# Optimization experiments

Hardware: AMD Instinct MI355X
Metric: run time of the kernel (lower is better)

## Reference

```python
import jax, jax.numpy as jnp
import numpy as np

N = 100_000   # nodes
E = 600_000   # edges
D = 128       # embed_dim
G = 1000      # graphs (batch ids)
L = 3         # num_layers


def setup_inputs() -> dict:
    key = jax.random.key(0)
    ks = jax.random.split(key, 12)
    s = 1.0 / np.sqrt(D)
    return {
        "x": jax.random.normal(ks[0], (N, D), jnp.float32),
        "edge_index": jax.random.randint(ks[1], (2, E), 0, N),
        "batch": jnp.sort(jax.random.randint(ks[2], (N,), 0, G)),
        "mask": jax.random.randint(ks[3], (N,), 0, 2),
        # stacked GCNConv weights/biases (in=hidden=out=D)
        "gcn_w": jax.random.normal(ks[4], (L, D, D), jnp.float32) * s,
        "gcn_b": jnp.zeros((L, D), jnp.float32),
        # MLP head: Linear(D,D) -> ReLU -> Linear(D,1)
        "lin1_w": jax.random.normal(ks[5], (D, D), jnp.float32) * s,
        "lin1_b": jnp.zeros((D,), jnp.float32),
        "lin2_w": jax.random.normal(ks[6], (D,), jnp.float32) * s,
        "lin2_b": jnp.zeros((), jnp.float32),
    }


def gcn_forward(x, src, dst, gcn_w, gcn_b):
    # symmetric gcn_norm with self-loops: deg[i] = 1 + in-degree(i)
    deg = jax.ops.segment_sum(jnp.ones((E,), x.dtype), dst, num_segments=N) + 1.0
    dinv = jax.lax.rsqrt(deg)
    enorm = dinv[src] * dinv[dst]          # [E] edge normalization
    self_norm = (dinv * dinv)[:, None]     # [N,1] self-loop normalization
    h = x
    for l in range(L):
        h = h @ gcn_w[l]                   # [N,D]
        h = (jax.ops.segment_sum(h[src] * enorm[:, None], dst, num_segments=N)
             + h * self_norm)
        h = h + gcn_b[l]
        if l < L - 1:
            h = jax.nn.relu(h)  # (dropout inactive at inference)
    return h


def reference(x, edge_index, batch, mask, gcn_w, gcn_b, lin1_w, lin1_b, lin2_w, lin2_b):
    src, dst = edge_index[0], edge_index[1]
    h = gcn_forward(x, src, dst, gcn_w, gcn_b)
    # MLP head -> per-node score [N]
    s = jax.nn.relu(h @ lin1_w + lin1_b) @ lin2_w + lin2_b
    s = jnp.where(mask == 0, jnp.float32(-1e9), s)
    # per-graph (segment) softmax — fused replacement for the unique/batch loop
    m = jax.ops.segment_max(s, batch, num_segments=G)
    e = jnp.exp(s - m[batch])
    z = jax.ops.segment_sum(e, batch, num_segments=G)
    return e / z[batch]
```

## Files before the change

kernel.cpp:

```cpp
#include <hip/hip_runtime.h>
#include <hip/hip_bf16.h>
#include <stdint.h>

typedef unsigned int u32;
typedef unsigned short u16;
typedef __attribute__((ext_vector_type(8))) short bf16x8;
typedef __attribute__((ext_vector_type(4))) float f32x4;

__device__ __forceinline__ float u16tof(u16 u){ return __uint_as_float(((u32)u) << 16); }
__device__ __forceinline__ float lo16(u32 v){ return __uint_as_float(v << 16); }
__device__ __forceinline__ float hi16(u32 v){ return __uint_as_float(v & 0xffff0000u); }
__device__ __forceinline__ u16 ftobf(float f){
  u32 b = __float_as_uint(f);
  return (u16)((b + 0x7FFFu + ((b >> 16) & 1u)) >> 16);
}
__device__ __forceinline__ u32 pack2(float a, float b){
  return (u32)ftobf(a) | ((u32)ftobf(b) << 16);
}
__device__ __forceinline__ float ldf(const void* p, int i, int isbf){
  return isbf ? u16tof(((const u16*)p)[i]) : ((const float*)p)[i];
}

__device__ __forceinline__ void acc8(float* a, uint4 v, float mk){
  a[0] = fmaf(lo16(v.x), mk, a[0]);
  a[1] = fmaf(hi16(v.x), mk, a[1]);
  a[2] = fmaf(lo16(v.y), mk, a[2]);
  a[3] = fmaf(hi16(v.y), mk, a[3]);
  a[4] = fmaf(lo16(v.z), mk, a[4]);
  a[5] = fmaf(hi16(v.z), mk, a[5]);
  a[6] = fmaf(lo16(v.w), mk, a[6]);
  a[7] = fmaf(hi16(v.w), mk, a[7]);
}

__device__ __forceinline__ void async16(const u16* g, const u16* l){
  __builtin_amdgcn_global_load_lds(
      (const __attribute__((address_space(1))) u32*)(uintptr_t)g,
      (__attribute__((address_space(3))) u32*)(uintptr_t)l,
      16, 0, 0);
}

__global__ __launch_bounds__(256) void k_prep(const void* __restrict__ gw, const void* __restrict__ l1w,
                                              const void* __restrict__ x, u16* __restrict__ Wf,
                                              u16* __restrict__ Hb, int L, int n8, int cvtB, int goffB,
                                              const int* __restrict__ batch, int* __restrict__ goff,
                                              int N, int G,
                                              const int* __restrict__ dst, int* __restrict__ hist,
                                              int nE, int chunk, int* __restrict__ flag){
  __shared__ int sh[256];
  const int b = blockIdx.x;
  const int t = threadIdx.x;
  const int histStart = L + 1 + cvtB + goffB;

  if (b >= histStart){
    sh[t] = 0; __syncthreads();
    const int blk = b - histStart;
    const int e0 = blk * chunk, e1 = min(e0 + chunk, nE);
    for (int e = e0 + t; e < e1; e += 256) atomicAdd(&sh[dst[e] >> 9], 1);
    __syncthreads();
    hist[blk * 256 + t] = sh[t];
    return;
  }
  if (b >= L + 1 + cvtB){
    const int i = (b - (L + 1 + cvtB)) * 256 + t;
    if (i >= N) return;
    const int bt = batch[i];
    const int prev = (i == 0) ? -1 : batch[i - 1];
    for (int g = prev + 1; g <= bt; ++g) goff[g] = i;
    if (i == N - 1){ for (int g = bt + 1; g <= G; ++g) goff[g] = N; }
    return;
  }
  if (t == 0) sh[0] = 0;
  __syncthreads();
  if (b <= L){
    int local = 0;
    for (int i = t; i < 4096; i += 256){
      u32 e = (((const u32*)gw)[i] >> 7) & 0xFFu;
      if (e >= 100u && e < 127u) local++;
    }
    atomicAdd(&sh[0], local);
    __syncthreads();
    const int isbf = (sh[0] > 2048) ? 1 : 0;
    if (b == 0 && t == 0) *flag = isbf;

    const void* src = (b < L) ? gw : l1w;
    const int sbase = (b < L) ? b * 16384 : 0;
    u16* dstp = Wf + (size_t)b * 16384;
    for (int g = t; g < 2048; g += 256){
      const int tt = g >> 8, ks = (g >> 6) & 3, lane = g & 63;
      const int n = tt * 16 + (lane & 15);
      const int k0 = ks * 32 + ((lane >> 4) << 3);
      u16* d = dstp + (size_t)g * 8;
      #pragma unroll
      for (int j = 0; j < 8; ++j){
        d[j] = ftobf(ldf(src, sbase + (k0 + j) * 128 + n, isbf));
      }
    }
  } else {
    u32 e = (((const u32*)gw)[t] >> 7) & 0xFFu;
    atomicAdd(&sh[0], (e >= 100u && e < 127u) ? 1 : 0);
    __syncthreads();
    if (sh[0] > 128) return;
    const int i = (b - (L + 1)) * 256 + t;
    if (i >= n8) return;
    const float4 a = ((const float4*)x)[i * 2];
    const float4 c = ((const float4*)x)[i * 2 + 1];
    u16* o = Hb + (size_t)i * 8;
    o[0] = ftobf(a.x); o[1] = ftobf(a.y); o[2] = ftobf(a.z); o[3] = ftobf(a.w);
    o[4] = ftobf(c.x); o[5] = ftobf(c.y); o[6] = ftobf(c.z); o[7] = ftobf(c.w);
  }
}

__global__ __launch_bounds__(256) void k_hscan(int* __restrict__ hist, int* __restrict__ bb, int nE){
  const int t = threadIdx.x;
  int run = 0;
  for (int j = 0; j < 256; j += 8){
    int v[8];
    #pragma unroll
    for (int k = 0; k < 8; ++k) v[k] = hist[(j + k) * 256 + t];
    #pragma unroll
    for (int k = 0; k < 8; ++k){
      hist[(j + k) * 256 + t] = run;
      run += v[k];
    }
  }
  __shared__ int sm[256];
  sm[t] = run; __syncthreads();
  for (int off = 1; off < 256; off <<= 1){
    int a = (t >= off) ? sm[t - off] : 0;
    __syncthreads();
    sm[t] += a;
    __syncthreads();
  }
  bb[t] = sm[t] - run;
  if (t == 255) bb[256] = nE;
}

__global__ __launch_bounds__(256) void k_scatter(const int* __restrict__ src, const int* __restrict__ dst,
                                                 const int* __restrict__ hist, const int* __restrict__ bb,
                                                 int2* __restrict__ tmpe, int nE, int chunk){
  __shared__ int base[256];
  const int blk = blockIdx.x, t = threadIdx.x;
  base[t] = bb[t] + hist[blk * 256 + t];
  __syncthreads();
  const int e0 = blk * chunk, e1 = min(e0 + chunk, nE);
  for (int e = e0 + t; e < e1; e += 256){
    const int d = dst[e];
    const int pos = atomicAdd(&base[d >> 9], 1);
    tmpe[pos] = make_int2(src[e], d);
  }
}

__global__ __launch_bounds__(256) void k_local(const int2* __restrict__ tmpe, const int* __restrict__ bb,
                                               int* __restrict__ boff, int* __restrict__ eid,
                                               float* __restrict__ dinv, int N, int nE, int nbkt){
  __shared__ int hcnt[512];
  __shared__ int hoff[512];
  const int b = blockIdx.x, t = threadIdx.x;
  const int n0 = b << 9;
  const int n1 = min(n0 + 512, N);
  const int nn = n1 - n0;
  const int e0 = bb[b], e1 = bb[b + 1];
  hcnt[t] = 0; hcnt[t + 256] = 0;
  __syncthreads();
  for (int e = e0 + t; e < e1; e += 256) atomicAdd(&hcnt[tmpe[e].y - n0], 1);
  __syncthreads();
  const int v0 = hcnt[t], v1 = hcnt[t + 256];
  hoff[t] = v0; hoff[t + 256] = v1;
  __syncthreads();
  for (int off = 1; off < 512; off <<= 1){
    int a0 = (t >= off) ? hoff[t - off] : 0;
    int a1 = (t + 256 >= off) ? hoff[t + 256 - off] : 0;
    __syncthreads();
    hoff[t] += a0; hoff[t + 256] += a1;
    __syncthreads();
  }
  const int ex0 = hoff[t] - v0 + e0;
  const int ex1 = hoff[t + 256] - v1 + e0;
  if (t < nn){       boff[n0 + t] = ex0;        dinv[n0 + t] = rsqrtf((float)v0 + 1.0f); }
  if (t + 256 < nn){ boff[n0 + t + 256] = ex1;  dinv[n0 + t + 256] = rsqrtf((float)v1 + 1.0f); }
  if (b == nbkt - 1 && t == 0) boff[N] = nE;
  __syncthreads();
  hoff[t] = ex0; hoff[t + 256] = ex1;
  __syncthreads();
  for (int e = e0 + t; e < e1; e += 256){
    const int2 pr = tmpe[e];
    const int pos = atomicAdd(&hoff[pr.y - n0], 1);
    eid[pos] = pr.x;
  }
}

__global__ __launch_bounds__(256) void k_mm(const void* __restrict__ X, const u16* __restrict__ Hb,
                                            const u16* __restrict__ Wf, const float* __restrict__ dinv,
                                            u16* __restrict__ T, int n, const int* __restrict__ fl){
  __shared__ u16 smw[16384];
  const int isbf = *fl;
  const u16* A = isbf ? (const u16*)X : Hb;
  {
    const uint4* s = (const uint4*)Wf;
    uint4* d = (uint4*)smw;
    for (int i = threadIdx.x; i < 2048; i += 256) d[i] = s[i];
  }
  __syncthreads();

  const int wave = threadIdx.x >> 6, lane = threadIdx.x & 63;
  const int m0 = blockIdx.x * 64 + wave * 16;
  int arow = m0 + (lane & 15); if (arow > n - 1) arow = n - 1;
  const u16* aptr = A + (size_t)arow * 128 + ((lane >> 4) << 3);

  f32x4 acc[8];
  #pragma unroll
  for (int t = 0; t < 8; ++t) acc[t] = (f32x4){0.f, 0.f, 0.f, 0.f};

  #pragma unroll
  for (int ks = 0; ks < 4; ++ks){
    const bf16x8 a = *(const bf16x8*)(aptr + ks * 32);
    #pragma unroll
    for (int t = 0; t < 8; ++t){
      const bf16x8 b = *(const bf16x8*)(smw + (size_t)(((t * 4 + ks) * 64 + lane) * 8));
      acc[t] = __builtin_amdgcn_mfma_f32_16x16x32_bf16(a, b, acc[t], 0, 0, 0);
    }
  }
  __syncthreads();

  const int quad = lane >> 4, col0 = lane & 15;
  float dv[4];
  #pragma unroll
  for (int r = 0; r < 4; ++r){
    const int row = m0 + quad * 4 + r;
    dv[r] = (row < n) ? dinv[row] : 0.f;
  }
  u16* my = smw + wave * 2112;
  #pragma unroll
  for (int t = 0; t < 8; ++t){
    #pragma unroll
    for (int r = 0; r < 4; ++r){
      my[(quad * 4 + r) * 132 + t * 16 + col0] = ftobf(acc[t][r] * dv[r]);
    }
  }
  #pragma unroll
  for (int i = 0; i < 4; ++i){
    const int row = i * 4 + (lane >> 4);
    const int grow = m0 + row;
    const int c8 = (lane & 15) * 8;
    if (grow < n){
      const u16* s = &my[row * 132 + c8];
      uint2 lo = *(const uint2*)(s);
      uint2 hi = *(const uint2*)(s + 4);
      *(uint4*)&T[(size_t)grow * 128 + c8] = make_uint4(lo.x, lo.y, hi.x, hi.y);
    }
  }
}

__device__ __forceinline__ void gather_ring(const u16* __restrict__ Tin, const int* __restrict__ eid,
                                            const int* __restrict__ seid, const int* __restrict__ sboff,
                                            int inlds, int e0, int wave, int lane, int sub, int l16,
                                            int js, int d, float* a){
  int T = 0;
  #pragma unroll
  for (int s = 0; s < 4; ++s){
    const int dd = sboff[wave * 4 + s + 1] - sboff[wave * 4 + s];
    T = (dd > T) ? dd : T;
  }
  if (T <= 0) return;

  if (inlds){
    extern __shared__ u16 dummy[];
    return;
  }
}

__global__ __launch_bounds__(256) void k_gmm(const u16* __restrict__ Tin, const int* __restrict__ boff,
                                             const int* __restrict__ eid, const float* __restrict__ dinv,
                                             const void* __restrict__ bias, int layer,
                                             const u16* __restrict__ Wf, u16* __restrict__ Tout,
                                             int n, const int* __restrict__ fl){
  __shared__ u16 sma[16 * 132];
  __shared__ u16 ring[4][4][512];
  __shared__ int seid[1024];
  __shared__ int sboff[17];
  const int isbf = *fl;
  const int tid = threadIdx.x;
  const int wave = tid >> 6, lane = tid & 63;
  const int sub = lane >> 4, l16 = lane & 15;
  const int m0 = blockIdx.x * 16;

  const int e0 = boff[m0];
  const int e1 = boff[min(m0 + 16, n)];
  const int len = e1 - e0;
  const int inlds = (len <= 1024);
  if (tid < 17) sboff[tid] = boff[min(m0 + tid, n)];
  if (inlds){ for (int i = tid; i < len; i += 256) seid[i] = eid[e0 + i]; }
  __syncthreads();

  const int wsub = wave * 4 + sub;
  const int node = m0 + wsub;
  const int js = sboff[wsub];
  const int d  = sboff[wsub + 1] - js;

  float a[8];
  #pragma unroll
  for (int k = 0; k < 8; ++k) a[k] = 0.f;
  if (node < n){
    const uint4 sv = ((const uint4*)(Tin + (size_t)node * 128))[l16];
    acc8(a, sv, 1.f);
  }

  int T = 0;
  #pragma unroll
  for (int s = 0; s < 4; ++s){
    const int dd = sboff[wave * 4 + s + 1] - sboff[wave * 4 + s];
    T = (dd > T) ? dd : T;
  }

  if (inlds){
    const int jloc = js - e0;
    const int jlast = jloc + ((d > 0) ? (d - 1) : 0);
    const u16* base = Tin + (size_t)l16 * 8;
    u16* slot = &ring[wave][0][0];
    #pragma unroll
    for (int t = 0; t < 4; ++t){
      if (t < T){
        const int idx = (d > 0) ? seid[(t < d) ? (jloc + t) : jlast] : 0;
        async16(base + (size_t)idx * 128, slot + (t & 3) * 512);
      }
    }
    int t = 0;
    for (; t + 4 <= T; ++t){
      asm volatile("s_waitcnt vmcnt(3)" ::: "memory");
      const uint4 v = *(const uint4*)(slot + (t & 3) * 512 + lane * 8);
      acc8(a, v, (t < d) ? 1.f : 0.f);
      const int tn = t + 4;
      if (tn < T){
        const int idx = (d > 0) ? seid[(tn < d) ? (jloc + tn) : jlast] : 0;
        async16(base + (size_t)idx * 128, slot + (tn & 3) * 512);
      }
    }
    for (; t < T; ++t){
      const int rem = T - t - 1;
      if (rem >= 2)      asm volatile("s_waitcnt vmcnt(2)" ::: "memory");
      else if (rem == 1) asm volatile("s_waitcnt vmcnt(1)" ::: "memory");
      else               asm volatile("s_waitcnt vmcnt(0)" ::: "memory");
      const uint4 v = *(const uint4*)(slot + (t & 3) * 512 + lane * 8);
      acc8(a, v, (t < d) ? 1.f : 0.f);
    }
  } else {
    for (int j = js; j < js + d; ++j){
      const uint4 v = ((const uint4*)(Tin + (size_t)eid[j] * 128))[l16];
      acc8(a, v, 1.f);
    }
  }

  float h[8];
  #pragma unroll
  for (int k = 0; k < 8; ++k) h[k] = 0.f;
  if (node < n){
    const float di = dinv[node];
    const int bb = layer * 128 + l16 * 8;
    #pragma unroll
    for (int k = 0; k < 8; ++k){
      h[k] = fmaxf(fmaf(a[k], di, ldf(bias, bb + k, isbf)), 0.f);
    }
  }
  {
    uint4 o;
    o.x = pack2(h[0], h[1]); o.y = pack2(h[2], h[3]); o.z = pack2(h[4], h[5]); o.w = pack2(h[6], h[7]);
    *(uint4*)&sma[(wave * 4 + sub) * 132 + l16 * 8] = o;
  }
  __syncthreads();

  f32x4 acc[2];
  acc[0] = (f32x4){0.f,0.f,0.f,0.f}; acc[1] = (f32x4){0.f,0.f,0.f,0.f};
  #pragma unroll
  for (int ks = 0; ks < 4; ++ks){
    const bf16x8 av = *(const bf16x8*)(sma + l16 * 132 + sub * 8 + ks * 32);
    #pragma unroll
    for (int tt = 0; tt < 2; ++tt){
      const int t = wave * 2 + tt;
      const bf16x8 bv = *(const bf16x8*)(Wf + (size_t)(((t * 4 + ks) * 64 + lane) * 8));
      acc[tt] = __builtin_amdgcn_mfma_f32_16x16x32_bf16(av, bv, acc[tt], 0, 0, 0);
    }
  }
  __syncthreads();

  float dv[4];
  #pragma unroll
  for (int r = 0; r < 4; ++r){
    const int row = m0 + sub * 4 + r;
    dv[r] = (row < n) ? dinv[row] : 0.f;
  }
  #pragma unroll
  for (int tt = 0; tt < 2; ++tt){
    const int t = wave * 2 + tt;
    #pragma unroll
    for (int r = 0; r < 4; ++r){
      sma[(sub * 4 + r) * 132 + t * 16 + l16] = ftobf(acc[tt][r] * dv[r]);
    }
  }
  __syncthreads();

  {
    const int row = tid >> 4;
    const int c8 = (tid & 15) * 8;
    if (m0 + row < n){
      const u16* s = &sma[row * 132 + c8];
      uint2 lo = *(const uint2*)(s);
      uint2 hi = *(const uint2*)(s + 4);
      *(uint4*)&Tout[(size_t)(m0 + row) * 128 + c8] = make_uint4(lo.x, lo.y, hi.x, hi.y);
    }
  }
}

__global__ __launch_bounds__(256) void k_ghead(const u16* __restrict__ Tin, const int* __restrict__ boff,
                                               const int* __restrict__ eid, const float* __restrict__ dinv,
                                               const void* __restrict__ bias, int layer,
                                               const u16* __restrict__ Wf, const void* __restrict__ b1,
                                               const void* __restrict__ w2, const void* __restrict__ b2,
                                               const int* __restrict__ mask, float* __restrict__ s,
                                               int n, const int* __restrict__ fl){
  __shared__ u16 sma[16 * 132];
  __shared__ u16 ring[4][4][512];
  __shared__ int seid[1024];
  __shared__ int sboff[17];
  __shared__ float sred[4][16];
  const int isbf = *fl;
  const int tid = threadIdx.x;
  const int wave = tid >> 6, lane = tid & 63;
  const int sub = lane >> 4, l16 = lane & 15;
  const int m0 = blockIdx.x * 16;

  const int e0 = boff[m0];
  const int e1 = boff[min(m0 + 16, n)];
  const int len = e1 - e0;
  const int inlds = (len <= 1024);
  if (tid < 17) sboff[tid] = boff[min(m0 + tid, n)];
  if (inlds){ for (int i = tid; i < len; i += 256) seid[i] = eid[e0 + i]; }
  __syncthreads();

  const int wsub = wave * 4 + sub;
  const int node = m0 + wsub;
  const int js = sboff[wsub];
  const int d  = sboff[wsub + 1] - js;

  float a[8];
  #pragma unroll
  for (int k = 0; k < 8; ++k) a[k] = 0.f;
  if (node < n){
    const uint4 sv = ((const uint4*)(Tin + (size_t)node * 128))[l16];
    acc8(a, sv, 1.f);
  }

  int T = 0;
  #pragma unroll
  for (int s2 = 0; s2 < 4; ++s2){
    const int dd = sboff[wave * 4 + s2 + 1] - sboff[wave * 4 + s2];
    T = (dd > T) ? dd : T;
  }

  if (inlds){
    const int jloc = js - e0;
    const int jlast = jloc + ((d > 0) ? (d - 1) : 0);
    const u16* base = Tin + (size_t)l16 * 8;
    u16* slot = &ring[wave][0][0];
    #pragma unroll
    for (int t = 0; t < 4; ++t){
      if (t < T){
        const int idx = (d > 0) ? seid[(t < d) ? (jloc + t) : jlast] : 0;
        async16(base + (size_t)idx * 128, slot + (t & 3) * 512);
      }
    }
    int t = 0;
    for (; t + 4 <= T; ++t){
      asm volatile("s_waitcnt vmcnt(3)" ::: "memory");
      const uint4 v = *(const uint4*)(slot + (t & 3) * 512 + lane * 8);
      acc8(a, v, (t < d) ? 1.f : 0.f);
      const int tn = t + 4;
      if (tn < T){
        const int idx = (d > 0) ? seid[(tn < d) ? (jloc + tn) : jlast] : 0;
        async16(base + (size_t)idx * 128, slot + (tn & 3) * 512);
      }
    }
    for (; t < T; ++t){
      const int rem = T - t - 1;
      if (rem >= 2)      asm volatile("s_waitcnt vmcnt(2)" ::: "memory");
      else if (rem == 1) asm volatile("s_waitcnt vmcnt(1)" ::: "memory");
      else               asm volatile("s_waitcnt vmcnt(0)" ::: "memory");
      const uint4 v = *(const uint4*)(slot + (t & 3) * 512 + lane * 8);
      acc8(a, v, (t < d) ? 1.f : 0.f);
    }
  } else {
    for (int j = js; j < js + d; ++j){
      const uint4 v = ((const uint4*)(Tin + (size_t)eid[j] * 128))[l16];
      acc8(a, v, 1.f);
    }
  }

  float h[8];
  #pragma unroll
  for (int k = 0; k < 8; ++k) h[k] = 0.f;
  if (node < n){
    const float di = dinv[node];
    const int bb = layer * 128 + l16 * 8;
    #pragma unroll
    for (int k = 0; k < 8; ++k){
      h[k] = fmaf(a[k], di, ldf(bias, bb + k, isbf));
    }
  }
  {
    uint4 o;
    o.x = pack2(h[0], h[1]); o.y = pack2(h[2], h[3]); o.z = pack2(h[4], h[5]); o.w = pack2(h[6], h[7]);
    *(uint4*)&sma[(wave * 4 + sub) * 132 + l16 * 8] = o;
  }
  __syncthreads();

  f32x4 acc[2];
  acc[0] = (f32x4){0.f,0.f,0.f,0.f}; acc[1] = (f32x4){0.f,0.f,0.f,0.f};
  #pragma unroll
  for (int ks = 0; ks < 4; ++ks){
    const bf16x8 av = *(const bf16x8*)(sma + l16 * 132 + sub * 8 + ks * 32);
    #pragma unroll
    for (int tt = 0; tt < 2; ++tt){
      const int t = wave * 2 + tt;
      const bf16x8 bv = *(const bf16x8*)(Wf + (size_t)(((t * 4 + ks) * 64 + lane) * 8));
      acc[tt] = __builtin_amdgcn_mfma_f32_16x16x32_bf16(av, bv, acc[tt], 0, 0, 0);
    }
  }

  float p0 = 0.f, p1 = 0.f, p2 = 0.f, p3 = 0.f;
  #pragma unroll
  for (int tt = 0; tt < 2; ++tt){
    const int col = (wave * 2 + tt) * 16 + l16;
    const float bv = ldf(b1, col, isbf);
    const float wv = ldf(w2, col, isbf);
    p0 = fmaf(fmaxf(acc[tt][0] + bv, 0.f), wv, p0);
    p1 = fmaf(fmaxf(acc[tt][1] + bv, 0.f), wv, p1);
    p2 = fmaf(fmaxf(acc[tt][2] + bv, 0.f), wv, p2);
    p3 = fmaf(fmaxf(acc[tt][3] + bv, 0.f), wv, p3);
  }
  #pragma unroll
  for (int k = 1; k < 16; k <<= 1){
    p0 += __shfl_xor(p0, k);
    p1 += __shfl_xor(p1, k);
    p2 += __shfl_xor(p2, k);
    p3 += __shfl_xor(p3, k);
  }
  if (l16 == 0){
    sred[wave][sub * 4 + 0] = p0;
    sred[wave][sub * 4 + 1] = p1;
    sred[wave][sub * 4 + 2] = p2;
    sred[wave][sub * 4 + 3] = p3;
  }
  __syncthreads();
  if (tid < 16){
    const int row = m0 + tid;
    if (row < n){
      float sc = sred[0][tid] + sred[1][tid] + sred[2][tid] + sred[3][tid]
               + ldf(b2, 0, isbf);
      if (mask[row] == 0) sc = -1e9f;
      s[row] = sc;
    }
  }
}

__global__ __launch_bounds__(256) void k_gsm(const float* __restrict__ s, const int* __restrict__ goff,
                                             void* __restrict__ out, int G, const int* __restrict__ fl){
  const int g = blockIdx.x * 4 + (threadIdx.x >> 6);
  if (g >= G) return;
  const int lane = threadIdx.x & 63;
  const int i0 = goff[g], i1 = goff[g + 1];
  if (i0 >= i1) return;
  float m = -3.4e38f;
  for (int j = i0 + lane; j < i1; j += 64) m = fmaxf(m, s[j]);
  #pragma unroll
  for (int k = 32; k; k >>= 1) m = fmaxf(m, __shfl_xor(m, k));
  float zz = 0.f;
  for (int j = i0 + lane; j < i1; j += 64) zz += expf(s[j] - m);
  #pragma unroll
  for (int k = 32; k; k >>= 1) zz += __shfl_xor(zz, k);
  const float rz = 1.f / zz;
  const int isbf = *fl;
  for (int j = i0 + lane; j < i1; j += 64){
    const float v = expf(s[j] - m) * rz;
    if (isbf) ((u16*)out)[j] = ftobf(v);
    else      ((float*)out)[j] = v;
  }
}

extern "C" void kernel_launch(void* const* d_in, const int* in_sizes, int n_in,
                              void* d_out, int out_size, void* d_ws, size_t ws_size,
                              hipStream_t stream){
  const void* x    = d_in[0];
  const int* ei    = (const int*)d_in[1];
  const int* batch = (const int*)d_in[2];
  const int* mask  = (const int*)d_in[3];
  const void* gw   = d_in[4];
  const void* gb   = d_in[5];
  const void* l1w  = d_in[6];
  const void* l1b  = d_in[7];
  const void* l2w  = d_in[8];
  const void* l2b  = d_in[9];

  const int N = in_sizes[2];
  const int E = in_sizes[1] / 2;
  const int D = 128;
  const int L = in_sizes[4] / (D * D);
  const int G = 1000;

  char* p = (char*)d_ws;
  u16*  Hb    = (u16*)p;   p += (size_t)N * D * sizeof(u16);
  u16*  Tb    = (u16*)p;   p += (size_t)N * D * sizeof(u16);
  u16*  Wf    = (u16*)p;   p += (size_t)(L + 1) * D * D * sizeof(u16);
  float* dinv = (float*)p; p += (size_t)N * sizeof(float);
  float* sbuf = (float*)p; p += (size_t)N * sizeof(float);
  int*  boff  = (int*)p;   p += (size_t)(N + 1) * sizeof(int);
  int*  eid   = (int*)p;   p += (size_t)E * sizeof(int);
  int*  goff  = (int*)p;   p += (size_t)(G + 1) * sizeof(int);
  int*  hist  = (int*)p;   p += 256 * 256 * sizeof(int);
  int*  bb    = (int*)p;   p += 260 * sizeof(int);
  int2* tmpe  = (int2*)p;  p += (size_t)E * sizeof(int2);
  int*  flag  = (int*)p;   p += 256;

  const int* srcp = ei;
  const int* dstp = ei + E;

  const int mmg   = (N + 63) / 64;
  const int fg    = (N + 15) / 16;
  const int n8    = N * D / 8;
  const int cvtB  = (n8 + 255) / 256;
  const int goffB = (N + 255) / 256;
  const int chunk = (E + 255) / 256;
  const int nbkt  = (N + 511) / 512;

  k_prep<<<(L + 1) + cvtB + goffB + 256, 256, 0, stream>>>(gw, l1w, x, Wf, Hb, L, n8, cvtB, goffB,
                                                           batch, goff, N, G, dstp, hist, E, chunk, flag);
  k_hscan<<<1, 256, 0, stream>>>(hist, bb, E);
  k_scatter<<<256, 256, 0, stream>>>(srcp, dstp, hist, bb, tmpe, E, chunk);
  k_local<<<nbkt, 256, 0, stream>>>(tmpe, bb, boff, eid, dinv, N, E, nbkt);

  k_mm<<<mmg, 256, 0, stream>>>(x, Hb, Wf, dinv, Tb, N, flag);
  k_gmm<<<fg, 256, 0, stream>>>(Tb, boff, eid, dinv, gb, 0, Wf + (size_t)1 * D * D, Hb, N, flag);
  k_gmm<<<fg, 256, 0, stream>>>(Hb, boff, eid, dinv, gb, 1, Wf + (size_t)2 * D * D, Tb, N, flag);
  k_ghead<<<fg, 256, 0, stream>>>(Tb, boff, eid, dinv, gb, 2, Wf + (size_t)L * D * D,
                                  l1b, l2w, l2b, mask, sbuf, N, flag);
  k_gsm<<<(G + 3) / 4, 256, 0, stream>>>(sbuf, goff, d_out, G, flag);
}
```

Before: 316.8 us.

## Split fused gather+matmul kernels into separate gather and matmul/head kernels

The gather-aggregate kernels no longer carry a 16-row MFMA matmul. They now write the aggregated hidden state to global memory, and the existing k_mm kernel is reused for the next layer's weight multiply. A new k_head kernel stages the full 128x128 weight in LDS and processes 64 rows per block for the MLP head. The aim is to free the gather kernel's LDS and registers for higher occupancy and to run the matmuls with better weight reuse. The cost is an extra N×D bf16 round trip through global memory and two more kernel launches per forward pass.

```diff
diff --git a/kernel.cpp b/kernel.cpp
--- a/kernel.cpp
+++ b/kernel.cpp
@@ -251,32 +251,12 @@
   }
 }
 
-__device__ __forceinline__ void gather_ring(const u16* __restrict__ Tin, const int* __restrict__ eid,
-                                            const int* __restrict__ seid, const int* __restrict__ sboff,
-                                            int inlds, int e0, int wave, int lane, int sub, int l16,
-                                            int js, int d, float* a){
-  int T = 0;
-  #pragma unroll
-  for (int s = 0; s < 4; ++s){
-    const int dd = sboff[wave * 4 + s + 1] - sboff[wave * 4 + s];
-    T = (dd > T) ? dd : T;
-  }
-  if (T <= 0) return;
-
-  if (inlds){
-    extern __shared__ u16 dummy[];
-    return;
-  }
-}
-
-__global__ __launch_bounds__(256) void k_gmm(const u16* __restrict__ Tin, const int* __restrict__ boff,
-                                             const int* __restrict__ eid, const float* __restrict__ dinv,
-                                             const void* __restrict__ bias, int layer,
-                                             const u16* __restrict__ Wf, u16* __restrict__ Tout,
-                                             int n, const int* __restrict__ fl){
-  __shared__ u16 sma[16 * 132];
+__global__ __launch_bounds__(256) void k_gath(const u16* __restrict__ Tin, const int* __restrict__ boff,
+                                              const int* __restrict__ eid, const float* __restrict__ dinv,
+                                              const void* __restrict__ bias, int layer, int dorelu,
+                                              u16* __restrict__ Hout, int n, const int* __restrict__ fl){
   __shared__ u16 ring[4][4][512];
-  __shared__ int seid[1024];
+  __shared__ int seid[512];
   __shared__ int sboff[17];
   const int isbf = *fl;
   const int tid = threadIdx.x;
@@ -287,7 +267,7 @@
   const int e0 = boff[m0];
   const int e1 = boff[min(m0 + 16, n)];
   const int len = e1 - e0;
-  const int inlds = (len <= 1024);
+  const int inlds = (len <= 512);
   if (tid < 17) sboff[tid] = boff[min(m0 + tid, n)];
   if (inlds){ for (int i = tid; i < len; i += 256) seid[i] = eid[e0 + i]; }
   __syncthreads();
@@ -307,8 +287,8 @@
 
   int T = 0;
   #pragma unroll
-  for (int s = 0; s < 4; ++s){
-    const int dd = sboff[wave * 4 + s + 1] - sboff[wave * 4 + s];
+  for (int s2 = 0; s2 < 4; ++s2){
+    const int dd = sboff[wave * 4 + s2 + 1] - sboff[wave * 4 + s2];
     T = (dd > T) ? dd : T;
   }
 
@@ -350,211 +330,80 @@
     }
   }
 
-  float h[8];
-  #pragma unroll
-  for (int k = 0; k < 8; ++k) h[k] = 0.f;
   if (node < n){
     const float di = dinv[node];
     const int bb = layer * 128 + l16 * 8;
+    float h[8];
     #pragma unroll
     for (int k = 0; k < 8; ++k){
-      h[k] = fmaxf(fmaf(a[k], di, ldf(bias, bb + k, isbf)), 0.f);
-    }
-  }
-  {
+      h[k] = fmaf(a[k], di, ldf(bias, bb + k, isbf));
+      if (dorelu) h[k] = fmaxf(h[k], 0.f);
+    }
     uint4 o;
     o.x = pack2(h[0], h[1]); o.y = pack2(h[2], h[3]); o.z = pack2(h[4], h[5]); o.w = pack2(h[6], h[7]);
-    *(uint4*)&sma[(wave * 4 + sub) * 132 + l16 * 8] = o;
-  }
-  __syncthreads();
-
-  f32x4 acc[2];
-  acc[0] = (f32x4){0.f,0.f,0.f,0.f}; acc[1] = (f32x4){0.f,0.f,0.f,0.f};
-  #pragma unroll
-  for (int ks = 0; ks < 4; ++ks){
-    const bf16x8 av = *(const bf16x8*)(sma + l16 * 132 + sub * 8 + ks * 32);
-    #pragma unroll
-    for (int tt = 0; tt < 2; ++tt){
-      const int t = wave * 2 + tt;
-      const bf16x8 bv = *(const bf16x8*)(Wf + (size_t)(((t * 4 + ks) * 64 + lane) * 8));
-      acc[tt] = __builtin_amdgcn_mfma_f32_16x16x32_bf16(av, bv, acc[tt], 0, 0, 0);
-    }
-  }
-  __syncthreads();
-
-  float dv[4];
-  #pragma unroll
-  for (int r = 0; r < 4; ++r){
-    const int row = m0 + sub * 4 + r;
-    dv[r] = (row < n) ? dinv[row] : 0.f;
-  }
-  #pragma unroll
-  for (int tt = 0; tt < 2; ++tt){
-    const int t = wave * 2 + tt;
-    #pragma unroll
-    for (int r = 0; r < 4; ++r){
-      sma[(sub * 4 + r) * 132 + t * 16 + l16] = ftobf(acc[tt][r] * dv[r]);
-    }
-  }
-  __syncthreads();
-
-  {
-    const int row = tid >> 4;
-    const int c8 = (tid & 15) * 8;
-    if (m0 + row < n){
-      const u16* s = &sma[row * 132 + c8];
-      uint2 lo = *(const uint2*)(s);
-      uint2 hi = *(const uint2*)(s + 4);
-      *(uint4*)&Tout[(size_t)(m0 + row) * 128 + c8] = make_uint4(lo.x, lo.y, hi.x, hi.y);
-    }
-  }
-}
-
-__global__ __launch_bounds__(256) void k_ghead(const u16* __restrict__ Tin, const int* __restrict__ boff,
-                                               const int* __restrict__ eid, const float* __restrict__ dinv,
-                                               const void* __restrict__ bias, int layer,
-                                               const u16* __restrict__ Wf, const void* __restrict__ b1,
-                                               const void* __restrict__ w2, const void* __restrict__ b2,
-                                               const int* __restrict__ mask, float* __restrict__ s,
-                                               int n, const int* __restrict__ fl){
-  __shared__ u16 sma[16 * 132];
-  __shared__ u16 ring[4][4][512];
-  __shared__ int seid[1024];
-  __shared__ int sboff[17];
+    *(uint4*)&Hout[(size_t)node * 128 + l16 * 8] = o;
+  }
+}
+
+__global__ __launch_bounds__(256) void k_head(const u16* __restrict__ H, const u16* __restrict__ Wf,
+                                              const void* __restrict__ b1, const void* __restrict__ w2,
+                                              const void* __restrict__ b2, const int* __restrict__ mask,
+                                              float* __restrict__ s, int n, const int* __restrict__ fl){
+  __shared__ u16 smw[16384];
   __shared__ float sred[4][16];
   const int isbf = *fl;
-  const int tid = threadIdx.x;
-  const int wave = tid >> 6, lane = tid & 63;
-  const int sub = lane >> 4, l16 = lane & 15;
-  const int m0 = blockIdx.x * 16;
-
-  const int e0 = boff[m0];
-  const int e1 = boff[min(m0 + 16, n)];
-  const int len = e1 - e0;
-  const int inlds = (len <= 1024);
-  if (tid < 17) sboff[tid] = boff[min(m0 + tid, n)];
-  if (inlds){ for (int i = tid; i < len; i += 256) seid[i] = eid[e0 + i]; }
-  __syncthreads();
-
-  const int wsub = wave * 4 + sub;
-  const int node = m0 + wsub;
-  const int js = sboff[wsub];
-  const int d  = sboff[wsub + 1] - js;
-
-  float a[8];
-  #pragma unroll
-  for (int k = 0; k < 8; ++k) a[k] = 0.f;
-  if (node < n){
-    const uint4 sv = ((const uint4*)(Tin + (size_t)node * 128))[l16];
-    acc8(a, sv, 1.f);
-  }
-
-  int T = 0;
-  #pragma unroll
-  for (int s2 = 0; s2 < 4; ++s2){
-    const int dd = sboff[wave * 4 + s2 + 1] - sboff[wave * 4 + s2];
-    T = (dd > T) ? dd : T;
-  }
-
-  if (inlds){
-    const int jloc = js - e0;
-    const int jlast = jloc + ((d > 0) ? (d - 1) : 0);
-    const u16* base = Tin + (size_t)l16 * 8;
-    u16* slot = &ring[wave][0][0];
-    #pragma unroll
-    for (int t = 0; t < 4; ++t){
-      if (t < T){
-        const int idx = (d > 0) ? seid[(t < d) ? (jloc + t) : jlast] : 0;
-        async16(base + (size_t)idx * 128, slot + (t & 3) * 512);
-      }
-    }
-    int t = 0;
-    for (; t + 4 <= T; ++t){
-      asm volatile("s_waitcnt vmcnt(3)" ::: "memory");
-      const uint4 v = *(const uint4*)(slot + (t & 3) * 512 + lane * 8);
-      acc8(a, v, (t < d) ? 1.f : 0.f);
-      const int tn = t + 4;
-      if (tn < T){
-        const int idx = (d > 0) ? seid[(tn < d) ? (jloc + tn) : jlast] : 0;
-        async16(base + (size_t)idx * 128, slot + (tn & 3) * 512);
-      }
-    }
-    for (; t < T; ++t){
-      const int rem = T - t - 1;
-      if (rem >= 2)      asm volatile("s_waitcnt vmcnt(2)" ::: "memory");
-      else if (rem == 1) asm volatile("s_waitcnt vmcnt(1)" ::: "memory");
-      else               asm volatile("s_waitcnt vmcnt(0)" ::: "memory");
-      const uint4 v = *(const uint4*)(slot + (t & 3) * 512 + lane * 8);
-      acc8(a, v, (t < d) ? 1.f : 0.f);
-    }
-  } else {
-    for (int j = js; j < js + d; ++j){
-      const uint4 v = ((const uint4*)(Tin + (size_t)eid[j] * 128))[l16];
-      acc8(a, v, 1.f);
-    }
-  }
-
-  float h[8];
-  #pragma unroll
-  for (int k = 0; k < 8; ++k) h[k] = 0.f;
-  if (node < n){
-    const float di = dinv[node];
-    const int bb = layer * 128 + l16 * 8;
-    #pragma unroll
-    for (int k = 0; k < 8; ++k){
-      h[k] = fmaf(a[k], di, ldf(bias, bb + k, isbf));
-    }
-  }
   {
-    uint4 o;
-    o.x = pack2(h[0], h[1]); o.y = pack2(h[2], h[3]); o.z = pack2(h[4], h[5]); o.w = pack2(h[6], h[7]);
-    *(uint4*)&sma[(wave * 4 + sub) * 132 + l16 * 8] = o;
-  }
-  __syncthreads();
-
-  f32x4 acc[2];
-  acc[0] = (f32x4){0.f,0.f,0.f,0.f}; acc[1] = (f32x4){0.f,0.f,0.f,0.f};
+    const uint4* sp = (const uint4*)Wf;
+    uint4* d = (uint4*)smw;
+    for (int i = threadIdx.x; i < 2048; i += 256) d[i] = sp[i];
+  }
+  __syncthreads();
+
+  const int wave = threadIdx.x >> 6, lane = threadIdx.x & 63;
+  const int m0 = blockIdx.x * 64 + wave * 16;
+  int arow = m0 + (lane & 15); if (arow > n - 1) arow = n - 1;
+  const u16* aptr = H + (size_t)arow * 128 + ((lane >> 4) << 3);
+
+  f32x4 acc[8];
+  #pragma unroll
+  for (int t = 0; t < 8; ++t) acc[t] = (f32x4){0.f, 0.f, 0.f, 0.f};
   #pragma unroll
   for (int ks = 0; ks < 4; ++ks){
-    const bf16x8 av = *(const bf16x8*)(sma + l16 * 132 + sub * 8 + ks * 32);
-    #pragma unroll
-    for (int tt = 0; tt < 2; ++tt){
-      const int t = wave * 2 + tt;
-      const bf16x8 bv = *(const bf16x8*)(Wf + (size_t)(((t * 4 + ks) * 64 + lane) * 8));
-      acc[tt] = __builtin_amdgcn_mfma_f32_16x16x32_bf16(av, bv, acc[tt], 0, 0, 0);
-    }
-  }
-
-  float p0 = 0.f, p1 = 0.f, p2 = 0.f, p3 = 0.f;
-  #pragma unroll
-  for (int tt = 0; tt < 2; ++tt){
-    const int col = (wave * 2 + tt) * 16 + l16;
+    const bf16x8 a = *(const bf16x8*)(aptr + ks * 32);
+    #pragma unroll
+    for (int t = 0; t < 8; ++t){
+      const bf16x8 b = *(const bf16x8*)(smw + (size_t)(((t * 4 + ks) * 64 + lane) * 8));
+      acc[t] = __builtin_amdgcn_mfma_f32_16x16x32_bf16(a, b, acc[t], 0, 0, 0);
+    }
+  }
+
+  const int quad = lane >> 4, col0 = lane & 15;
+  float p[4] = {0.f, 0.f, 0.f, 0.f};
+  #pragma unroll
+  for (int t = 0; t < 8; ++t){
+    const int col = t * 16 + col0;
     const float bv = ldf(b1, col, isbf);
     const float wv = ldf(w2, col, isbf);
-    p0 = fmaf(fmaxf(acc[tt][0] + bv, 0.f), wv, p0);
-    p1 = fmaf(fmaxf(acc[tt][1] + bv, 0.f), wv, p1);
-    p2 = fmaf(fmaxf(acc[tt][2] + bv, 0.f), wv, p2);
-    p3 = fmaf(fmaxf(acc[tt][3] + bv, 0.f), wv, p3);
+    #pragma unroll
+    for (int r = 0; r < 4; ++r){
+      p[r] = fmaf(fmaxf(acc[t][r] + bv, 0.f), wv, p[r]);
+    }
   }
   #pragma unroll
   for (int k = 1; k < 16; k <<= 1){
-    p0 += __shfl_xor(p0, k);
-    p1 += __shfl_xor(p1, k);
-    p2 += __shfl_xor(p2, k);
-    p3 += __shfl_xor(p3, k);
-  }
-  if (l16 == 0){
-    sred[wave][sub * 4 + 0] = p0;
-    sred[wave][sub * 4 + 1] = p1;
-    sred[wave][sub * 4 + 2] = p2;
-    sred[wave][sub * 4 + 3] = p3;
-  }
-  __syncthreads();
-  if (tid < 16){
-    const int row = m0 + tid;
+    #pragma unroll
+    for (int r = 0; r < 4; ++r) p[r] += __shfl_xor(p[r], k);
+  }
+  if (col0 == 0){
+    #pragma unroll
+    for (int r = 0; r < 4; ++r) sred[wave][quad * 4 + r] = p[r];
+  }
+  __syncthreads();
+  if (threadIdx.x < 64){
+    const int row = blockIdx.x * 64 + threadIdx.x;
     if (row < n){
-      float sc = sred[0][tid] + sred[1][tid] + sred[2][tid] + sred[3][tid]
-               + ldf(b2, 0, isbf);
+      const int w = threadIdx.x >> 4, idx = threadIdx.x & 15;
+      float sc = sred[w][idx] + ldf(b2, 0, isbf);
       if (mask[row] == 0) sc = -1e9f;
       s[row] = sc;
     }
@@ -637,9 +486,11 @@
   k_local<<<nbkt, 256, 0, stream>>>(tmpe, bb, boff, eid, dinv, N, E, nbkt);
 
   k_mm<<<mmg, 256, 0, stream>>>(x, Hb, Wf, dinv, Tb, N, flag);
-  k_gmm<<<fg, 256, 0, stream>>>(Tb, boff, eid, dinv, gb, 0, Wf + (size_t)1 * D * D, Hb, N, flag);
-  k_gmm<<<fg, 256, 0, stream>>>(Hb, boff, eid, dinv, gb, 1, Wf + (size_t)2 * D * D, Tb, N, flag);
-  k_ghead<<<fg, 256, 0, stream>>>(Tb, boff, eid, dinv, gb, 2, Wf + (size_t)L * D * D,
-                                  l1b, l2w, l2b, mask, sbuf, N, flag);
+  k_gath<<<fg, 256, 0, stream>>>(Tb, boff, eid, dinv, gb, 0, 1, Hb, N, flag);
+  k_mm<<<mmg, 256, 0, stream>>>(Hb, Hb, Wf + (size_t)1 * D * D, dinv, Tb, N, flag);
+  k_gath<<<fg, 256, 0, stream>>>(Tb, boff, eid, dinv, gb, 1, 1, Hb, N, flag);
+  k_mm<<<mmg, 256, 0, stream>>>(Hb, Hb, Wf + (size_t)2 * D * D, dinv, Tb, N, flag);
+  k_gath<<<fg, 256, 0, stream>>>(Tb, boff, eid, dinv, gb, 2, 0, Hb, N, flag);
+  k_head<<<mmg, 256, 0, stream>>>(Hb, Wf + (size_t)L * D * D, l1b, l2w, l2b, mask, sbuf, N, flag);
   k_gsm<<<(G + 3) / 4, 256, 0, stream>>>(sbuf, goff, d_out, G, flag);
 }
```

After: 325.8 us. 1.03x slower.

## Fuse fp32-to-bf16 input conversion into first matmul and parallelize histogram scan

Applied to the files above, without the earlier changes.

Removes the separate pass that converted x from fp32 to bf16 in k_prep. k_mm now loads fp32 rows directly and rounds them to bf16 in registers, which saves writing and re-reading a full N×D bf16 buffer. The single-block k_hscan is replaced by a 256-block k_hsum that scans each bucket's column. The small bucket-sum prefix scan is then recomputed redundantly inside k_scatter and k_local, which adds a little per-block work in exchange for removing a serial single-block kernel.

```diff
diff --git a/kernel.cpp b/kernel.cpp
--- a/kernel.cpp
+++ b/kernel.cpp
@@ -40,8 +40,7 @@
 }
 
 __global__ __launch_bounds__(256) void k_prep(const void* __restrict__ gw, const void* __restrict__ l1w,
-                                              const void* __restrict__ x, u16* __restrict__ Wf,
-                                              u16* __restrict__ Hb, int L, int n8, int cvtB, int goffB,
+                                              u16* __restrict__ Wf, int L, int goffB,
                                               const int* __restrict__ batch, int* __restrict__ goff,
                                               int N, int G,
                                               const int* __restrict__ dst, int* __restrict__ hist,
@@ -49,7 +48,7 @@
   __shared__ int sh[256];
   const int b = blockIdx.x;
   const int t = threadIdx.x;
-  const int histStart = L + 1 + cvtB + goffB;
+  const int histStart = L + 1 + goffB;
 
   if (b >= histStart){
     sh[t] = 0; __syncthreads();
@@ -60,8 +59,8 @@
     hist[blk * 256 + t] = sh[t];
     return;
   }
-  if (b >= L + 1 + cvtB){
-    const int i = (b - (L + 1 + cvtB)) * 256 + t;
+  if (b >= L + 1){
+    const int i = (b - (L + 1)) * 256 + t;
     if (i >= N) return;
     const int bt = batch[i];
     const int prev = (i == 0) ? -1 : batch[i - 1];
@@ -71,76 +70,62 @@
   }
   if (t == 0) sh[0] = 0;
   __syncthreads();
-  if (b <= L){
-    int local = 0;
-    for (int i = t; i < 4096; i += 256){
-      u32 e = (((const u32*)gw)[i] >> 7) & 0xFFu;
-      if (e >= 100u && e < 127u) local++;
-    }
-    atomicAdd(&sh[0], local);
-    __syncthreads();
-    const int isbf = (sh[0] > 2048) ? 1 : 0;
-    if (b == 0 && t == 0) *flag = isbf;
-
-    const void* src = (b < L) ? gw : l1w;
-    const int sbase = (b < L) ? b * 16384 : 0;
-    u16* dstp = Wf + (size_t)b * 16384;
-    for (int g = t; g < 2048; g += 256){
-      const int tt = g >> 8, ks = (g >> 6) & 3, lane = g & 63;
-      const int n = tt * 16 + (lane & 15);
-      const int k0 = ks * 32 + ((lane >> 4) << 3);
-      u16* d = dstp + (size_t)g * 8;
-      #pragma unroll
-      for (int j = 0; j < 8; ++j){
-        d[j] = ftobf(ldf(src, sbase + (k0 + j) * 128 + n, isbf));
-      }
-    }
-  } else {
-    u32 e = (((const u32*)gw)[t] >> 7) & 0xFFu;
-    atomicAdd(&sh[0], (e >= 100u && e < 127u) ? 1 : 0);
-    __syncthreads();
-    if (sh[0] > 128) return;
-    const int i = (b - (L + 1)) * 256 + t;
-    if (i >= n8) return;
-    const float4 a = ((const float4*)x)[i * 2];
-    const float4 c = ((const float4*)x)[i * 2 + 1];
-    u16* o = Hb + (size_t)i * 8;
-    o[0] = ftobf(a.x); o[1] = ftobf(a.y); o[2] = ftobf(a.z); o[3] = ftobf(a.w);
-    o[4] = ftobf(c.x); o[5] = ftobf(c.y); o[6] = ftobf(c.z); o[7] = ftobf(c.w);
-  }
-}
-
-__global__ __launch_bounds__(256) void k_hscan(int* __restrict__ hist, int* __restrict__ bb, int nE){
+  int local = 0;
+  for (int i = t; i < 4096; i += 256){
+    u32 e = (((const u32*)gw)[i] >> 7) & 0xFFu;
+    if (e >= 100u && e < 127u) local++;
+  }
+  atomicAdd(&sh[0], local);
+  __syncthreads();
+  const int isbf = (sh[0] > 2048) ? 1 : 0;
+  if (b == 0 && t == 0) *flag = isbf;
+
+  const void* src = (b < L) ? gw : l1w;
+  const int sbase = (b < L) ? b * 16384 : 0;
+  u16* dstp = Wf + (size_t)b * 16384;
+  for (int g = t; g < 2048; g += 256){
+    const int tt = g >> 8, ks = (g >> 6) & 3, lane = g & 63;
+    const int n = tt * 16 + (lane & 15);
+    const int k0 = ks * 32 + ((lane >> 4) << 3);
+    u16* d = dstp + (size_t)g * 8;
+    #pragma unroll
+    for (int j = 0; j < 8; ++j){
+      d[j] = ftobf(ldf(src, sbase + (k0 + j) * 128 + n, isbf));
+    }
+  }
+}
+
+__global__ __launch_bounds__(256) void k_hsum(int* __restrict__ hist, int* __restrict__ bsum){
+  __shared__ int sm[256];
+  const int b = blockIdx.x;
   const int t = threadIdx.x;
-  int run = 0;
-  for (int j = 0; j < 256; j += 8){
-    int v[8];
-    #pragma unroll
-    for (int k = 0; k < 8; ++k) v[k] = hist[(j + k) * 256 + t];
-    #pragma unroll
-    for (int k = 0; k < 8; ++k){
-      hist[(j + k) * 256 + t] = run;
-      run += v[k];
-    }
-  }
-  __shared__ int sm[256];
-  sm[t] = run; __syncthreads();
+  const int v = hist[t * 256 + b];
+  sm[t] = v; __syncthreads();
   for (int off = 1; off < 256; off <<= 1){
     int a = (t >= off) ? sm[t - off] : 0;
     __syncthreads();
     sm[t] += a;
     __syncthreads();
   }
-  bb[t] = sm[t] - run;
-  if (t == 255) bb[256] = nE;
+  hist[t * 256 + b] = sm[t] - v;
+  if (t == 255) bsum[b] = sm[255];
 }
 
 __global__ __launch_bounds__(256) void k_scatter(const int* __restrict__ src, const int* __restrict__ dst,
-                                                 const int* __restrict__ hist, const int* __restrict__ bb,
+                                                 const int* __restrict__ hist, const int* __restrict__ bsum,
                                                  int2* __restrict__ tmpe, int nE, int chunk){
+  __shared__ int sm[256];
   __shared__ int base[256];
   const int blk = blockIdx.x, t = threadIdx.x;
-  base[t] = bb[t] + hist[blk * 256 + t];
+  const int v = bsum[t];
+  sm[t] = v; __syncthreads();
+  for (int off = 1; off < 256; off <<= 1){
+    int a = (t >= off) ? sm[t - off] : 0;
+    __syncthreads();
+    sm[t] += a;
+    __syncthreads();
+  }
+  base[t] = (sm[t] - v) + hist[blk * 256 + t];
   __syncthreads();
   const int e0 = blk * chunk, e1 = min(e0 + chunk, nE);
   for (int e = e0 + t; e < e1; e += 256){
@@ -150,16 +135,31 @@
   }
 }
 
-__global__ __launch_bounds__(256) void k_local(const int2* __restrict__ tmpe, const int* __restrict__ bb,
+__global__ __launch_bounds__(256) void k_local(const int2* __restrict__ tmpe, const int* __restrict__ bsum,
                                                int* __restrict__ boff, int* __restrict__ eid,
                                                float* __restrict__ dinv, int N, int nE, int nbkt){
+  __shared__ int sm[256];
+  __shared__ int bbx[257];
   __shared__ int hcnt[512];
   __shared__ int hoff[512];
   const int b = blockIdx.x, t = threadIdx.x;
+  {
+    const int v = bsum[t];
+    sm[t] = v; __syncthreads();
+    for (int off = 1; off < 256; off <<= 1){
+      int a = (t >= off) ? sm[t - off] : 0;
+      __syncthreads();
+      sm[t] += a;
+      __syncthreads();
+    }
+    bbx[t] = sm[t] - v;
+    if (t == 255) bbx[256] = sm[255];
+  }
+  __syncthreads();
   const int n0 = b << 9;
   const int n1 = min(n0 + 512, N);
   const int nn = n1 - n0;
-  const int e0 = bb[b], e1 = bb[b + 1];
+  const int e0 = bbx[b], e1 = bbx[b + 1];
   hcnt[t] = 0; hcnt[t + 256] = 0;
   __syncthreads();
   for (int e = e0 + t; e < e1; e += 256) atomicAdd(&hcnt[tmpe[e].y - n0], 1);
@@ -189,12 +189,12 @@
   }
 }
 
-__global__ __launch_bounds__(256) void k_mm(const void* __restrict__ X, const u16* __restrict__ Hb,
-                                            const u16* __restrict__ Wf, const float* __restrict__ dinv,
-                                            u16* __restrict__ T, int n, const int* __restrict__ fl){
+__global__ __launch_bounds__(256) void k_mm(const void* __restrict__ X, const u16* __restrict__ Wf,
+                                            const float* __restrict__ dinv, u16* __restrict__ T,
+                                            int n, int cvtin, const int* __restrict__ fl){
   __shared__ u16 smw[16384];
   const int isbf = *fl;
-  const u16* A = isbf ? (const u16*)X : Hb;
+  const int fp32in = cvtin && !isbf;
   {
     const uint4* s = (const uint4*)Wf;
     uint4* d = (uint4*)smw;
@@ -205,7 +205,7 @@
   const int wave = threadIdx.x >> 6, lane = threadIdx.x & 63;
   const int m0 = blockIdx.x * 64 + wave * 16;
   int arow = m0 + (lane & 15); if (arow > n - 1) arow = n - 1;
-  const u16* aptr = A + (size_t)arow * 128 + ((lane >> 4) << 3);
+  const int koff = (lane >> 4) << 3;
 
   f32x4 acc[8];
   #pragma unroll
@@ -213,7 +213,16 @@
 
   #pragma unroll
   for (int ks = 0; ks < 4; ++ks){
-    const bf16x8 a = *(const bf16x8*)(aptr + ks * 32);
+    bf16x8 a;
+    if (fp32in){
+      const float* ap = (const float*)X + (size_t)arow * 128 + koff + ks * 32;
+      const float4 f0 = *(const float4*)ap;
+      const float4 f1 = *(const float4*)(ap + 4);
+      a = (bf16x8){(short)ftobf(f0.x), (short)ftobf(f0.y), (short)ftobf(f0.z), (short)ftobf(f0.w),
+                   (short)ftobf(f1.x), (short)ftobf(f1.y), (short)ftobf(f1.z), (short)ftobf(f1.w)};
+    } else {
+      a = *(const bf16x8*)((const u16*)X + (size_t)arow * 128 + koff + ks * 32);
+    }
     #pragma unroll
     for (int t = 0; t < 8; ++t){
       const bf16x8 b = *(const bf16x8*)(smw + (size_t)(((t * 4 + ks) * 64 + lane) * 8));
@@ -248,24 +257,6 @@
       uint2 hi = *(const uint2*)(s + 4);
       *(uint4*)&T[(size_t)grow * 128 + c8] = make_uint4(lo.x, lo.y, hi.x, hi.y);
     }
-  }
-}
-
-__device__ __forceinline__ void gather_ring(const u16* __restrict__ Tin, const int* __restrict__ eid,
-                                            const int* __restrict__ seid, const int* __restrict__ sboff,
-                                            int inlds, int e0, int wave, int lane, int sub, int l16,
-                                            int js, int d, float* a){
-  int T = 0;
-  #pragma unroll
-  for (int s = 0; s < 4; ++s){
-    const int dd = sboff[wave * 4 + s + 1] - sboff[wave * 4 + s];
-    T = (dd > T) ? dd : T;
-  }
-  if (T <= 0) return;
-
-  if (inlds){
-    extern __shared__ u16 dummy[];
-    return;
   }
 }
 
@@ -307,8 +298,8 @@
 
   int T = 0;
   #pragma unroll
-  for (int s = 0; s < 4; ++s){
-    const int dd = sboff[wave * 4 + s + 1] - sboff[wave * 4 + s];
+  for (int s2 = 0; s2 < 4; ++s2){
+    const int dd = sboff[wave * 4 + s2 + 1] - sboff[wave * 4 + s2];
     T = (dd > T) ? dd : T;
   }
 
@@ -615,7 +606,7 @@
   int*  eid   = (int*)p;   p += (size_t)E * sizeof(int);
   int*  goff  = (int*)p;   p += (size_t)(G + 1) * sizeof(int);
   int*  hist  = (int*)p;   p += 256 * 256 * sizeof(int);
-  int*  bb    = (int*)p;   p += 260 * sizeof(int);
+  int*  bsum  = (int*)p;   p += 256 * sizeof(int);
   int2* tmpe  = (int2*)p;  p += (size_t)E * sizeof(int2);
   int*  flag  = (int*)p;   p += 256;
 
@@ -624,19 +615,17 @@
 
   const int mmg   = (N + 63) / 64;
   const int fg    = (N + 15) / 16;
-  const int n8    = N * D / 8;
-  const int cvtB  = (n8 + 255) / 256;
   const int goffB = (N + 255) / 256;
   const int chunk = (E + 255) / 256;
   const int nbkt  = (N + 511) / 512;
 
-  k_prep<<<(L + 1) + cvtB + goffB + 256, 256, 0, stream>>>(gw, l1w, x, Wf, Hb, L, n8, cvtB, goffB,
-                                                           batch, goff, N, G, dstp, hist, E, chunk, flag);
-  k_hscan<<<1, 256, 0, stream>>>(hist, bb, E);
-  k_scatter<<<256, 256, 0, stream>>>(srcp, dstp, hist, bb, tmpe, E, chunk);
-  k_local<<<nbkt, 256, 0, stream>>>(tmpe, bb, boff, eid, dinv, N, E, nbkt);
-
-  k_mm<<<mmg, 256, 0, stream>>>(x, Hb, Wf, dinv, Tb, N, flag);
+  k_prep<<<(L + 1) + goffB + 256, 256, 0, stream>>>(gw, l1w, Wf, L, goffB,
+                                                    batch, goff, N, G, dstp, hist, E, chunk, flag);
+  k_hsum<<<256, 256, 0, stream>>>(hist, bsum);
+  k_scatter<<<256, 256, 0, stream>>>(srcp, dstp, hist, bsum, tmpe, E, chunk);
+  k_local<<<nbkt, 256, 0, stream>>>(tmpe, bsum, boff, eid, dinv, N, E, nbkt);
+
+  k_mm<<<mmg, 256, 0, stream>>>(x, Wf, dinv, Tb, N, 1, flag);
   k_gmm<<<fg, 256, 0, stream>>>(Tb, boff, eid, dinv, gb, 0, Wf + (size_t)1 * D * D, Hb, N, flag);
   k_gmm<<<fg, 256, 0, stream>>>(Hb, boff, eid, dinv, gb, 1, Wf + (size_t)2 * D * D, Tb, N, flag);
   k_ghead<<<fg, 256, 0, stream>>>(Tb, boff, eid, dinv, gb, 2, Wf + (size_t)L * D * D,
```

Measured after the change: 312.8 us, median of 2. No clear change (-1.3%).
